# Kernel optimization log

Hardware: AMD Instinct MI355X
Metric: run time of the kernel (lower is better)

## Reference

```python
import jax, jax.numpy as jnp
import numpy as np

N_CLUSTERS = 1024


def setup_inputs() -> dict:
    key = jax.random.key(0)
    k1, k2 = jax.random.split(key)
    batch = jax.random.normal(k1, (262144, 64), dtype=jnp.float32)
    centroids = jax.random.normal(k2, (N_CLUSTERS, 64), dtype=jnp.float32)
    return {"batch": batch, "centroids": centroids}


def reference(batch, centroids):
    x_sq = jnp.sum(batch * batch, axis=1, keepdims=True)          # [N, 1]
    c_sq = jnp.sum(centroids * centroids, axis=1)                 # [K]
    cross = batch @ centroids.T                                   # [N, K]
    distances = x_sq - 2.0 * cross + c_sq[None, :]
    assignments = jnp.argmin(distances, axis=1)                   # [N] int
    # Counts and sums via scatter-add (avoids materializing one-hot [N, K])
    batch_cluster_counts = jnp.zeros((N_CLUSTERS,), dtype=jnp.int32).at[assignments].add(1)
    batch_cluster_sums = jax.ops.segment_sum(batch, assignments, num_segments=N_CLUSTERS)  # [K, D]
    return (assignments, batch_cluster_counts, batch_cluster_sums)
```

## Files before the change

kernel.cpp:

```cpp
#include <hip/hip_runtime.h>
#include <float.h>

#define N_PTS 262144
#define K_CL  1024
#define D     64
#define PTS_PER_WAVE   64
#define WAVES_PER_BLK  16
#define PTS_PER_BLK    (PTS_PER_WAVE * WAVES_PER_BLK)
#define NTILE 8
#define MARGIN_S 0.5f
#define CAND_CAP 6

typedef _Float16 f16;
typedef _Float16 half8 __attribute__((ext_vector_type(8)));
typedef float    f32x4 __attribute__((ext_vector_type(4)));

__global__ __launch_bounds__(256) void prep_kernel(const float* __restrict__ cent,
                                                   float* __restrict__ csq,
                                                   float* __restrict__ csqhn,
                                                   f16* __restrict__ cent16) {
    int k = blockIdx.x * 256 + threadIdx.x;
    if (k >= K_CL) return;
    const float* row = &cent[(size_t)k * D];
    float s = 0.f;
    #pragma unroll
    for (int d = 0; d < D; ++d) s = fmaf(row[d], row[d], s);
    csq[k]   = s;
    csqhn[k] = -0.5f * s;
    int sw = k & 7;
    #pragma unroll
    for (int ch = 0; ch < 8; ++ch) {
        half8 h;
        #pragma unroll
        for (int e = 0; e < 8; ++e) h[e] = (f16)row[ch * 8 + e];
        *reinterpret_cast<half8*>(&cent16[(size_t)k * D + (size_t)((ch ^ sw) * 8)]) = h;
    }
}

__device__ __forceinline__ float exact_dist(const float* __restrict__ xr,
                                            const float* __restrict__ cr,
                                            float xsq, float cs) {
    float dot = 0.f;
    #pragma unroll
    for (int d = 0; d < D; ++d) dot = fmaf(xr[d], cr[d], dot);
    return (xsq - 2.0f * dot) + cs;
}

__device__ __forceinline__ half8 point_frag(const float* __restrict__ batch,
                                            int prow, int chunk) {
    const float* src = &batch[(size_t)prow * D + chunk * 8];
    float4 u0 = *reinterpret_cast<const float4*>(src);
    float4 u1 = *reinterpret_cast<const float4*>(src + 4);
    half8 h;
    h[0] = (f16)u0.x; h[1] = (f16)u0.y; h[2] = (f16)u0.z; h[3] = (f16)u0.w;
    h[4] = (f16)u1.x; h[5] = (f16)u1.y; h[6] = (f16)u1.z; h[7] = (f16)u1.w;
    return h;
}

__device__ __forceinline__ float vmax4(const f32x4& a) {
    return fmaxf(fmaxf(a.x, a.y), fmaxf(a.z, a.w));
}

__device__ __forceinline__ void collect(const f32x4& a, float thr, int cbase, int& cnt,
                                        int& s0, int& s1, int& s2, int& s3, int& s4, int& s5) {
    if (vmax4(a) >= thr) {
        #pragma unroll
        for (int r = 0; r < 4; ++r) {
            if (a[r] >= thr) {
                int c = cbase + r;
                if      (cnt == 0) s0 = c;
                else if (cnt == 1) s1 = c;
                else if (cnt == 2) s2 = c;
                else if (cnt == 3) s3 = c;
                else if (cnt == 4) s4 = c;
                else if (cnt == 5) s5 = c;
                cnt++;
            }
        }
    }
}

__device__ __forceinline__ void resolve(const float* __restrict__ batch,
                                        const float* __restrict__ cent,
                                        const float* __restrict__ csq,
                                        int prow, int hi, int cnt,
                                        int s0, int s1, int s2, int s3, int s4, int s5,
                                        float& bd, int& bi) {
    bd = FLT_MAX; bi = 0x7fffffff;
    if (cnt == 0) return;
    const float* xr = &batch[(size_t)prow * D];
    float xsq = 0.f;
    #pragma unroll
    for (int d = 0; d < D; ++d) xsq = fmaf(xr[d], xr[d], xsq);
    if (cnt <= CAND_CAP) {
        #pragma unroll
        for (int r = 0; r < CAND_CAP; ++r) {
            int c = (r == 0) ? s0 : (r == 1) ? s1 : (r == 2) ? s2
                  : (r == 3) ? s3 : (r == 4) ? s4 : s5;
            if (r < cnt) {
                float dd = exact_dist(xr, &cent[(size_t)c * D], xsq, csq[c]);
                if (dd < bd || (dd == bd && c < bi)) { bd = dd; bi = c; }
            }
        }
    } else {
        for (int t16 = 0; t16 < 64; ++t16) {
            #pragma unroll
            for (int r = 0; r < 4; ++r) {
                int c = t16 * 16 + hi * 4 + r;
                float dd = exact_dist(xr, &cent[(size_t)c * D], xsq, csq[c]);
                if (dd < bd || (dd == bd && c < bi)) { bd = dd; bi = c; }
            }
        }
    }
}

__global__ __launch_bounds__(1024, 4) void assign_kernel(
    const float* __restrict__ batch,
    const f16*   __restrict__ cent16,
    const float* __restrict__ csq,
    const float* __restrict__ csqhn,
    const float* __restrict__ cent,
    float* __restrict__ out_assign,
    float* __restrict__ ps_base,
    float* __restrict__ cs_base,
    int split_mask)
{
    __shared__ f16   C16[K_CL * D];
    __shared__ __align__(16) float CH[K_CL];

    const int tid   = threadIdx.x;
    const int wave  = tid >> 6;
    const int lane  = tid & 63;
    const int lo    = lane & 15;
    const int hi    = lane >> 4;
    const int wbase = (blockIdx.x * WAVES_PER_BLK + wave) * PTS_PER_WAVE;

    #pragma unroll
    for (int it = 0; it < 8; ++it) {
        int u = tid + 1024 * it;
        *reinterpret_cast<half8*>(&C16[u * 8]) =
            *reinterpret_cast<const half8*>(&cent16[(size_t)u * 8]);
    }
    CH[tid] = csqhn[tid];
    __syncthreads();

    const int pr0 = wbase + 0 * 16 + lo;
    const int pr1 = wbase + 1 * 16 + lo;
    const int pr2 = wbase + 2 * 16 + lo;
    const int pr3 = wbase + 3 * 16 + lo;

    const half8 p0a = point_frag(batch, pr0, hi), p0b = point_frag(batch, pr0, 4 + hi);
    const half8 p1a = point_frag(batch, pr1, hi), p1b = point_frag(batch, pr1, 4 + hi);
    const half8 p2a = point_frag(batch, pr2, hi), p2b = point_frag(batch, pr2, 4 + hi);
    const half8 p3a = point_frag(batch, pr3, hi), p3b = point_frag(batch, pr3, 4 + hi);

    float m0 = -FLT_MAX, m1 = -FLT_MAX, m2 = -FLT_MAX, m3 = -FLT_MAX;
    for (int t = 0; t < NTILE; ++t) {
        const int base = t * 128;
        #pragma unroll
        for (int m = 0; m < 8; ++m) {
            const int row = base + m * 16 + lo;
            const int sw  = row & 7;
            const half8 cf0 = *reinterpret_cast<const half8*>(&C16[row * D + ((hi     ^ sw) * 8)]);
            const half8 cf1 = *reinterpret_cast<const half8*>(&C16[row * D + (((4+hi) ^ sw) * 8)]);
            const f32x4 ch  = *reinterpret_cast<const f32x4*>(&CH[base + m * 16 + hi * 4]);
            f32x4 a0 = ch, a1 = ch, a2 = ch, a3 = ch;
            a0 = __builtin_amdgcn_mfma_f32_16x16x32_f16(cf0, p0a, a0, 0, 0, 0);
            a0 = __builtin_amdgcn_mfma_f32_16x16x32_f16(cf1, p0b, a0, 0, 0, 0);
            a1 = __builtin_amdgcn_mfma_f32_16x16x32_f16(cf0, p1a, a1, 0, 0, 0);
            a1 = __builtin_amdgcn_mfma_f32_16x16x32_f16(cf1, p1b, a1, 0, 0, 0);
            a2 = __builtin_amdgcn_mfma_f32_16x16x32_f16(cf0, p2a, a2, 0, 0, 0);
            a2 = __builtin_amdgcn_mfma_f32_16x16x32_f16(cf1, p2b, a2, 0, 0, 0);
            a3 = __builtin_amdgcn_mfma_f32_16x16x32_f16(cf0, p3a, a3, 0, 0, 0);
            a3 = __builtin_amdgcn_mfma_f32_16x16x32_f16(cf1, p3b, a3, 0, 0, 0);
            m0 = fmaxf(m0, vmax4(a0));
            m1 = fmaxf(m1, vmax4(a1));
            m2 = fmaxf(m2, vmax4(a2));
            m3 = fmaxf(m3, vmax4(a3));
        }
    }
    m0 = fmaxf(m0, __shfl_xor(m0, 16)); m0 = fmaxf(m0, __shfl_xor(m0, 32));
    m1 = fmaxf(m1, __shfl_xor(m1, 16)); m1 = fmaxf(m1, __shfl_xor(m1, 32));
    m2 = fmaxf(m2, __shfl_xor(m2, 16)); m2 = fmaxf(m2, __shfl_xor(m2, 32));
    m3 = fmaxf(m3, __shfl_xor(m3, 16)); m3 = fmaxf(m3, __shfl_xor(m3, 32));
    const float t0 = m0 - MARGIN_S, t1 = m1 - MARGIN_S,
                t2 = m2 - MARGIN_S, t3 = m3 - MARGIN_S;

    int n0 = 0, n1 = 0, n2 = 0, n3 = 0;
    int a0c0=0,a0c1=0,a0c2=0,a0c3=0,a0c4=0,a0c5=0;
    int a1c0=0,a1c1=0,a1c2=0,a1c3=0,a1c4=0,a1c5=0;
    int a2c0=0,a2c1=0,a2c2=0,a2c3=0,a2c4=0,a2c5=0;
    int a3c0=0,a3c1=0,a3c2=0,a3c3=0,a3c4=0,a3c5=0;

    for (int t = 0; t < NTILE; ++t) {
        const int base = t * 128;
        #pragma unroll
        for (int m = 0; m < 8; ++m) {
            const int row = base + m * 16 + lo;
            const int sw  = row & 7;
            const half8 cf0 = *reinterpret_cast<const half8*>(&C16[row * D + ((hi     ^ sw) * 8)]);
            const half8 cf1 = *reinterpret_cast<const half8*>(&C16[row * D + (((4+hi) ^ sw) * 8)]);
            const f32x4 ch  = *reinterpret_cast<const f32x4*>(&CH[base + m * 16 + hi * 4]);
            f32x4 a0 = ch, a1 = ch, a2 = ch, a3 = ch;
            a0 = __builtin_amdgcn_mfma_f32_16x16x32_f16(cf0, p0a, a0, 0, 0, 0);
            a0 = __builtin_amdgcn_mfma_f32_16x16x32_f16(cf1, p0b, a0, 0, 0, 0);
            a1 = __builtin_amdgcn_mfma_f32_16x16x32_f16(cf0, p1a, a1, 0, 0, 0);
            a1 = __builtin_amdgcn_mfma_f32_16x16x32_f16(cf1, p1b, a1, 0, 0, 0);
            a2 = __builtin_amdgcn_mfma_f32_16x16x32_f16(cf0, p2a, a2, 0, 0, 0);
            a2 = __builtin_amdgcn_mfma_f32_16x16x32_f16(cf1, p2b, a2, 0, 0, 0);
            a3 = __builtin_amdgcn_mfma_f32_16x16x32_f16(cf0, p3a, a3, 0, 0, 0);
            a3 = __builtin_amdgcn_mfma_f32_16x16x32_f16(cf1, p3b, a3, 0, 0, 0);
            const int cbase = base + m * 16 + hi * 4;
            collect(a0, t0, cbase, n0, a0c0, a0c1, a0c2, a0c3, a0c4, a0c5);
            collect(a1, t1, cbase, n1, a1c0, a1c1, a1c2, a1c3, a1c4, a1c5);
            collect(a2, t2, cbase, n2, a2c0, a2c1, a2c2, a2c3, a2c4, a2c5);
            collect(a3, t3, cbase, n3, a3c0, a3c1, a3c2, a3c3, a3c4, a3c5);
        }
    }

    float bd0, bd1, bd2, bd3;
    int   bi0, bi1, bi2, bi3;
    resolve(batch, cent, csq, pr0, hi, n0, a0c0, a0c1, a0c2, a0c3, a0c4, a0c5, bd0, bi0);
    resolve(batch, cent, csq, pr1, hi, n1, a1c0, a1c1, a1c2, a1c3, a1c4, a1c5, bd1, bi1);
    resolve(batch, cent, csq, pr2, hi, n2, a2c0, a2c1, a2c2, a2c3, a2c4, a2c5, bd2, bi2);
    resolve(batch, cent, csq, pr3, hi, n3, a3c0, a3c1, a3c2, a3c3, a3c4, a3c5, bd3, bi3);

    #pragma unroll
    for (int off = 16; off <= 32; off <<= 1) {
        float od; int oi;
        od = __shfl_xor(bd0, off); oi = __shfl_xor(bi0, off);
        if (od < bd0 || (od == bd0 && oi < bi0)) { bd0 = od; bi0 = oi; }
        od = __shfl_xor(bd1, off); oi = __shfl_xor(bi1, off);
        if (od < bd1 || (od == bd1 && oi < bi1)) { bd1 = od; bi1 = oi; }
        od = __shfl_xor(bd2, off); oi = __shfl_xor(bi2, off);
        if (od < bd2 || (od == bd2 && oi < bi2)) { bd2 = od; bi2 = oi; }
        od = __shfl_xor(bd3, off); oi = __shfl_xor(bi3, off);
        if (od < bd3 || (od == bd3 && oi < bi3)) { bd3 = od; bi3 = oi; }
    }

    if (hi == 0) {
        out_assign[pr0] = (float)bi0;
        out_assign[pr1] = (float)bi1;
        out_assign[pr2] = (float)bi2;
        out_assign[pr3] = (float)bi3;
    }

    const int split = (blockIdx.x * WAVES_PER_BLK + wave) & split_mask;
    float* ps = ps_base + (size_t)split * K_CL * D;
    float* cs = cs_base + (size_t)split * K_CL;
    #pragma unroll 4
    for (int s = 0; s < 4; ++s) {
        int bis = (s == 0) ? bi0 : (s == 1) ? bi1 : (s == 2) ? bi2 : bi3;
        for (int p = 0; p < 16; ++p) {
            int a = __shfl(bis, p);
            int pt = wbase + s * 16 + p;
            float v = batch[(size_t)pt * D + lane];
            atomicAdd(&ps[(size_t)a * D + lane], v);
            if (lane == 0) atomicAdd(&cs[a], 1.0f);
        }
    }
}

__global__ __launch_bounds__(256) void reduce_kernel(
    const float* __restrict__ partial,
    const float* __restrict__ cnt_partial,
    float* __restrict__ out_counts,
    float* __restrict__ out_sums,
    int nsplit)
{
    int idx = blockIdx.x * 256 + threadIdx.x;
    if (idx < K_CL * D) {
        float s = 0.f;
        for (int e = 0; e < nsplit; ++e) s += partial[(size_t)e * K_CL * D + idx];
        out_sums[idx] = s;
    } else if (idx < K_CL * D + K_CL) {
        int c = idx - K_CL * D;
        float s = 0.f;
        for (int e = 0; e < nsplit; ++e) s += cnt_partial[e * K_CL + c];
        out_counts[c] = s;
    }
}

extern "C" void kernel_launch(void* const* d_in, const int* in_sizes, int n_in,
                              void* d_out, int out_size, void* d_ws, size_t ws_size,
                              hipStream_t stream) {
    const float* batch = (const float*)d_in[0];
    const float* cent  = (const float*)d_in[1];
    float* out        = (float*)d_out;
    float* out_assign = out;
    float* out_counts = out + N_PTS;
    float* out_sums   = out + N_PTS + K_CL;

    char* ws = (char*)d_ws;
    float* csq    = (float*)ws;
    float* csqhn  = (float*)(ws + 4096);
    f16*   cent16 = (f16*)(ws + 8192);
    float* partial = (float*)(ws + 8192 + 131072);

    int nsplit = 0;
    for (int ns = 32; ns >= 2; ns >>= 1) {
        size_t need = 8192 + 131072 +
                      (size_t)ns * K_CL * D * 4 + (size_t)ns * K_CL * 4;
        if (ws_size >= need) { nsplit = ns; break; }
    }

    prep_kernel<<<K_CL / 256, 256, 0, stream>>>(cent, csq, csqhn, cent16);

    if (nsplit > 0) {
        float* cnt_partial = partial + (size_t)nsplit * K_CL * D;
        hipMemsetAsync(partial, 0,
                       (size_t)(nsplit * K_CL * D + nsplit * K_CL) * sizeof(float), stream);
        assign_kernel<<<N_PTS / PTS_PER_BLK, 1024, 0, stream>>>(
            batch, cent16, csq, csqhn, cent, out_assign,
            partial, cnt_partial, nsplit - 1);
        reduce_kernel<<<(K_CL * D + K_CL + 255) / 256, 256, 0, stream>>>(
            partial, cnt_partial, out_counts, out_sums, nsplit);
    } else {
        hipMemsetAsync(out_counts, 0, (size_t)(K_CL + K_CL * D) * sizeof(float), stream);
        assign_kernel<<<N_PTS / PTS_PER_BLK, 1024, 0, stream>>>(
            batch, cent16, csq, csqhn, cent, out_assign,
            out_sums, out_counts, 0);
    }
}
```

Before: 191.0 us.

## Fuse max and candidate passes into one MFMA sweep with running top-4

```diff
diff --git a/kernel.cpp b/kernel.cpp
--- a/kernel.cpp
+++ b/kernel.cpp
@@ -9,7 +9,7 @@
 #define PTS_PER_BLK    (PTS_PER_WAVE * WAVES_PER_BLK)
 #define NTILE 8
 #define MARGIN_S 0.5f
-#define CAND_CAP 6
+#define CAP 4
 
 typedef _Float16 f16;
 typedef _Float16 half8 __attribute__((ext_vector_type(8)));
@@ -61,42 +61,50 @@
     return fmaxf(fmaxf(a.x, a.y), fmaxf(a.z, a.w));
 }
 
-__device__ __forceinline__ void collect(const f32x4& a, float thr, int cbase, int& cnt,
-                                        int& s0, int& s1, int& s2, int& s3, int& s4, int& s5) {
-    if (vmax4(a) >= thr) {
-        #pragma unroll
-        for (int r = 0; r < 4; ++r) {
-            if (a[r] >= thr) {
-                int c = cbase + r;
-                if      (cnt == 0) s0 = c;
-                else if (cnt == 1) s1 = c;
-                else if (cnt == 2) s2 = c;
-                else if (cnt == 3) s3 = c;
-                else if (cnt == 4) s4 = c;
-                else if (cnt == 5) s5 = c;
-                cnt++;
-            }
-        }
-    }
-}
-
-__device__ __forceinline__ void resolve(const float* __restrict__ batch,
-                                        const float* __restrict__ cent,
-                                        const float* __restrict__ csq,
-                                        int prow, int hi, int cnt,
-                                        int s0, int s1, int s2, int s3, int s4, int s5,
-                                        float& bd, int& bi) {
+__device__ __forceinline__ void rins(float sv, int c, int& cnt,
+                                     float& s0, float& s1, float& s2, float& s3,
+                                     int& i0, int& i1, int& i2, int& i3) {
+    if (cnt < CAP) {
+        if      (cnt == 0) { s0 = sv; i0 = c; }
+        else if (cnt == 1) { s1 = sv; i1 = c; }
+        else if (cnt == 2) { s2 = sv; i2 = c; }
+        else               { s3 = sv; i3 = c; }
+        cnt++;
+    } else {
+        float mn = s0; int mi = 0;
+        if (s1 < mn) { mn = s1; mi = 1; }
+        if (s2 < mn) { mn = s2; mi = 2; }
+        if (s3 < mn) { mn = s3; mi = 3; }
+        if (sv > mn) {
+            if      (mi == 0) { s0 = sv; i0 = c; }
+            else if (mi == 1) { s1 = sv; i1 = c; }
+            else if (mi == 2) { s2 = sv; i2 = c; }
+            else              { s3 = sv; i3 = c; }
+        }
+    }
+}
+
+__device__ __forceinline__ void resolve_r(const float* __restrict__ batch,
+                                          const float* __restrict__ cent,
+                                          const float* __restrict__ csq,
+                                          int prow, int hi, float thrF, int cnt,
+                                          float s0, float s1, float s2, float s3,
+                                          int i0, int i1, int i2, int i3,
+                                          float& bd, int& bi) {
     bd = FLT_MAX; bi = 0x7fffffff;
-    if (cnt == 0) return;
     const float* xr = &batch[(size_t)prow * D];
     float xsq = 0.f;
     #pragma unroll
     for (int d = 0; d < D; ++d) xsq = fmaf(xr[d], xr[d], xsq);
-    if (cnt <= CAND_CAP) {
+    int svc = 0;
+    if (cnt > 0 && s0 >= thrF) svc++;
+    if (cnt > 1 && s1 >= thrF) svc++;
+    if (cnt > 2 && s2 >= thrF) svc++;
+    if (cnt > 3 && s3 >= thrF) svc++;
+    if (svc < CAP) {
         #pragma unroll
-        for (int r = 0; r < CAND_CAP; ++r) {
-            int c = (r == 0) ? s0 : (r == 1) ? s1 : (r == 2) ? s2
-                  : (r == 3) ? s3 : (r == 4) ? s4 : s5;
+        for (int r = 0; r < CAP; ++r) {
+            int c = (r == 0) ? i0 : (r == 1) ? i1 : (r == 2) ? i2 : i3;
             if (r < cnt) {
                 float dd = exact_dist(xr, &cent[(size_t)c * D], xsq, csq[c]);
                 if (dd < bd || (dd == bd && c < bi)) { bd = dd; bi = c; }
@@ -155,42 +163,11 @@
     const half8 p3a = point_frag(batch, pr3, hi), p3b = point_frag(batch, pr3, 4 + hi);
 
     float m0 = -FLT_MAX, m1 = -FLT_MAX, m2 = -FLT_MAX, m3 = -FLT_MAX;
-    for (int t = 0; t < NTILE; ++t) {
-        const int base = t * 128;
-        #pragma unroll
-        for (int m = 0; m < 8; ++m) {
-            const int row = base + m * 16 + lo;
-            const int sw  = row & 7;
-            const half8 cf0 = *reinterpret_cast<const half8*>(&C16[row * D + ((hi     ^ sw) * 8)]);
-            const half8 cf1 = *reinterpret_cast<const half8*>(&C16[row * D + (((4+hi) ^ sw) * 8)]);
-            const f32x4 ch  = *reinterpret_cast<const f32x4*>(&CH[base + m * 16 + hi * 4]);
-            f32x4 a0 = ch, a1 = ch, a2 = ch, a3 = ch;
-            a0 = __builtin_amdgcn_mfma_f32_16x16x32_f16(cf0, p0a, a0, 0, 0, 0);
-            a0 = __builtin_amdgcn_mfma_f32_16x16x32_f16(cf1, p0b, a0, 0, 0, 0);
-            a1 = __builtin_amdgcn_mfma_f32_16x16x32_f16(cf0, p1a, a1, 0, 0, 0);
-            a1 = __builtin_amdgcn_mfma_f32_16x16x32_f16(cf1, p1b, a1, 0, 0, 0);
-            a2 = __builtin_amdgcn_mfma_f32_16x16x32_f16(cf0, p2a, a2, 0, 0, 0);
-            a2 = __builtin_amdgcn_mfma_f32_16x16x32_f16(cf1, p2b, a2, 0, 0, 0);
-            a3 = __builtin_amdgcn_mfma_f32_16x16x32_f16(cf0, p3a, a3, 0, 0, 0);
-            a3 = __builtin_amdgcn_mfma_f32_16x16x32_f16(cf1, p3b, a3, 0, 0, 0);
-            m0 = fmaxf(m0, vmax4(a0));
-            m1 = fmaxf(m1, vmax4(a1));
-            m2 = fmaxf(m2, vmax4(a2));
-            m3 = fmaxf(m3, vmax4(a3));
-        }
-    }
-    m0 = fmaxf(m0, __shfl_xor(m0, 16)); m0 = fmaxf(m0, __shfl_xor(m0, 32));
-    m1 = fmaxf(m1, __shfl_xor(m1, 16)); m1 = fmaxf(m1, __shfl_xor(m1, 32));
-    m2 = fmaxf(m2, __shfl_xor(m2, 16)); m2 = fmaxf(m2, __shfl_xor(m2, 32));
-    m3 = fmaxf(m3, __shfl_xor(m3, 16)); m3 = fmaxf(m3, __shfl_xor(m3, 32));
-    const float t0 = m0 - MARGIN_S, t1 = m1 - MARGIN_S,
-                t2 = m2 - MARGIN_S, t3 = m3 - MARGIN_S;
-
-    int n0 = 0, n1 = 0, n2 = 0, n3 = 0;
-    int a0c0=0,a0c1=0,a0c2=0,a0c3=0,a0c4=0,a0c5=0;
-    int a1c0=0,a1c1=0,a1c2=0,a1c3=0,a1c4=0,a1c5=0;
-    int a2c0=0,a2c1=0,a2c2=0,a2c3=0,a2c4=0,a2c5=0;
-    int a3c0=0,a3c1=0,a3c2=0,a3c3=0,a3c4=0,a3c5=0;
+    int   n0 = 0, n1 = 0, n2 = 0, n3 = 0;
+    float s00=0,s01=0,s02=0,s03=0, s10=0,s11=0,s12=0,s13=0;
+    float s20=0,s21=0,s22=0,s23=0, s30=0,s31=0,s32=0,s33=0;
+    int   i00=0,i01=0,i02=0,i03=0, i10=0,i11=0,i12=0,i13=0;
+    int   i20=0,i21=0,i22=0,i23=0, i30=0,i31=0,i32=0,i33=0;
 
     for (int t = 0; t < NTILE; ++t) {
         const int base = t * 128;
@@ -211,19 +188,62 @@
             a3 = __builtin_amdgcn_mfma_f32_16x16x32_f16(cf0, p3a, a3, 0, 0, 0);
             a3 = __builtin_amdgcn_mfma_f32_16x16x32_f16(cf1, p3b, a3, 0, 0, 0);
             const int cbase = base + m * 16 + hi * 4;
-            collect(a0, t0, cbase, n0, a0c0, a0c1, a0c2, a0c3, a0c4, a0c5);
-            collect(a1, t1, cbase, n1, a1c0, a1c1, a1c2, a1c3, a1c4, a1c5);
-            collect(a2, t2, cbase, n2, a2c0, a2c1, a2c2, a2c3, a2c4, a2c5);
-            collect(a3, t3, cbase, n3, a3c0, a3c1, a3c2, a3c3, a3c4, a3c5);
-        }
-    }
+
+            float mx;
+            mx = vmax4(a0); m0 = fmaxf(m0, mx);
+            if (mx >= m0 - MARGIN_S) {
+                #pragma unroll
+                for (int r = 0; r < 4; ++r) {
+                    float sv = a0[r];
+                    if (sv >= m0 - MARGIN_S)
+                        rins(sv, cbase + r, n0, s00, s01, s02, s03, i00, i01, i02, i03);
+                }
+            }
+            mx = vmax4(a1); m1 = fmaxf(m1, mx);
+            if (mx >= m1 - MARGIN_S) {
+                #pragma unroll
+                for (int r = 0; r < 4; ++r) {
+                    float sv = a1[r];
+                    if (sv >= m1 - MARGIN_S)
+                        rins(sv, cbase + r, n1, s10, s11, s12, s13, i10, i11, i12, i13);
+                }
+            }
+            mx = vmax4(a2); m2 = fmaxf(m2, mx);
+            if (mx >= m2 - MARGIN_S) {
+                #pragma unroll
+                for (int r = 0; r < 4; ++r) {
+                    float sv = a2[r];
+                    if (sv >= m2 - MARGIN_S)
+                        rins(sv, cbase + r, n2, s20, s21, s22, s23, i20, i21, i22, i23);
+                }
+            }
+            mx = vmax4(a3); m3 = fmaxf(m3, mx);
+            if (mx >= m3 - MARGIN_S) {
+                #pragma unroll
+                for (int r = 0; r < 4; ++r) {
+                    float sv = a3[r];
+                    if (sv >= m3 - MARGIN_S)
+                        rins(sv, cbase + r, n3, s30, s31, s32, s33, i30, i31, i32, i33);
+                }
+            }
+        }
+    }
+
+    m0 = fmaxf(m0, __shfl_xor(m0, 16)); m0 = fmaxf(m0, __shfl_xor(m0, 32));
+    m1 = fmaxf(m1, __shfl_xor(m1, 16)); m1 = fmaxf(m1, __shfl_xor(m1, 32));
+    m2 = fmaxf(m2, __shfl_xor(m2, 16)); m2 = fmaxf(m2, __shfl_xor(m2, 32));
+    m3 = fmaxf(m3, __shfl_xor(m3, 16)); m3 = fmaxf(m3, __shfl_xor(m3, 32));
 
     float bd0, bd1, bd2, bd3;
     int   bi0, bi1, bi2, bi3;
-    resolve(batch, cent, csq, pr0, hi, n0, a0c0, a0c1, a0c2, a0c3, a0c4, a0c5, bd0, bi0);
-    resolve(batch, cent, csq, pr1, hi, n1, a1c0, a1c1, a1c2, a1c3, a1c4, a1c5, bd1, bi1);
-    resolve(batch, cent, csq, pr2, hi, n2, a2c0, a2c1, a2c2, a2c3, a2c4, a2c5, bd2, bi2);
-    resolve(batch, cent, csq, pr3, hi, n3, a3c0, a3c1, a3c2, a3c3, a3c4, a3c5, bd3, bi3);
+    resolve_r(batch, cent, csq, pr0, hi, m0 - MARGIN_S, n0,
+              s00, s01, s02, s03, i00, i01, i02, i03, bd0, bi0);
+    resolve_r(batch, cent, csq, pr1, hi, m1 - MARGIN_S, n1,
+              s10, s11, s12, s13, i10, i11, i12, i13, bd1, bi1);
+    resolve_r(batch, cent, csq, pr2, hi, m2 - MARGIN_S, n2,
+              s20, s21, s22, s23, i20, i21, i22, i23, bd2, bi2);
+    resolve_r(batch, cent, csq, pr3, hi, m3 - MARGIN_S, n3,
+              s30, s31, s32, s33, i30, i31, i32, i33, bd3, bi3);
 
     #pragma unroll
     for (int off = 16; off <= 32; off <<= 1) {
@@ -308,7 +328,7 @@
 
     if (nsplit > 0) {
         float* cnt_partial = partial + (size_t)nsplit * K_CL * D;
-        hipMemsetAsync(partial, 0,
+        (void)hipMemsetAsync(partial, 0,
                        (size_t)(nsplit * K_CL * D + nsplit * K_CL) * sizeof(float), stream);
         assign_kernel<<<N_PTS / PTS_PER_BLK, 1024, 0, stream>>>(
             batch, cent16, csq, csqhn, cent, out_assign,
@@ -316,7 +336,7 @@
         reduce_kernel<<<(K_CL * D + K_CL + 255) / 256, 256, 0, stream>>>(
             partial, cnt_partial, out_counts, out_sums, nsplit);
     } else {
-        hipMemsetAsync(out_counts, 0, (size_t)(K_CL + K_CL * D) * sizeof(float), stream);
+        (void)hipMemsetAsync(out_counts, 0, (size_t)(K_CL + K_CL * D) * sizeof(float), stream);
         assign_kernel<<<N_PTS / PTS_PER_BLK, 1024, 0, stream>>>(
             batch, cent16, csq, csqhn, cent, out_assign,
             out_sums, out_counts, 0);
```

Measured after the change: 658.9 us. +245.0%, slower.

## Move cluster sum scatter into separate LDS-accumulating kernel, drop split partials

Applied to the files above, without the earlier changes.

```diff
diff --git a/kernel.cpp b/kernel.cpp
--- a/kernel.cpp
+++ b/kernel.cpp
@@ -10,6 +10,8 @@
 #define NTILE 8
 #define MARGIN_S 0.5f
 #define CAND_CAP 6
+#define SBLK 64
+#define PPB  (N_PTS / SBLK)
 
 typedef _Float16 f16;
 typedef _Float16 half8 __attribute__((ext_vector_type(8)));
@@ -120,10 +122,7 @@
     const float* __restrict__ csq,
     const float* __restrict__ csqhn,
     const float* __restrict__ cent,
-    float* __restrict__ out_assign,
-    float* __restrict__ ps_base,
-    float* __restrict__ cs_base,
-    int split_mask)
+    float* __restrict__ out_assign)
 {
     __shared__ f16   C16[K_CL * D];
     __shared__ __align__(16) float CH[K_CL];
@@ -244,41 +243,83 @@
         out_assign[pr2] = (float)bi2;
         out_assign[pr3] = (float)bi3;
     }
-
-    const int split = (blockIdx.x * WAVES_PER_BLK + wave) & split_mask;
-    float* ps = ps_base + (size_t)split * K_CL * D;
-    float* cs = cs_base + (size_t)split * K_CL;
-    #pragma unroll 4
-    for (int s = 0; s < 4; ++s) {
-        int bis = (s == 0) ? bi0 : (s == 1) ? bi1 : (s == 2) ? bi2 : bi3;
-        for (int p = 0; p < 16; ++p) {
-            int a = __shfl(bis, p);
-            int pt = wbase + s * 16 + p;
-            float v = batch[(size_t)pt * D + lane];
-            atomicAdd(&ps[(size_t)a * D + lane], v);
-            if (lane == 0) atomicAdd(&cs[a], 1.0f);
-        }
-    }
-}
-
-__global__ __launch_bounds__(256) void reduce_kernel(
-    const float* __restrict__ partial,
-    const float* __restrict__ cnt_partial,
+}
+
+__global__ __launch_bounds__(1024) void scatter_lds_kernel(
+    const float* __restrict__ batch,
+    const float* __restrict__ assignF,
     float* __restrict__ out_counts,
-    float* __restrict__ out_sums,
-    int nsplit)
+    float* __restrict__ out_sums)
 {
-    int idx = blockIdx.x * 256 + threadIdx.x;
-    if (idx < K_CL * D) {
-        float s = 0.f;
-        for (int e = 0; e < nsplit; ++e) s += partial[(size_t)e * K_CL * D + idx];
-        out_sums[idx] = s;
-    } else if (idx < K_CL * D + K_CL) {
-        int c = idx - K_CL * D;
-        float s = 0.f;
-        for (int e = 0; e < nsplit; ++e) s += cnt_partial[e * K_CL + c];
-        out_counts[c] = s;
-    }
+    __shared__ f16 S16[K_CL * D];
+    __shared__ int acnt[K_CL];
+    __shared__ int a_lds[PPB];
+
+    const int tid  = threadIdx.x;
+    const int wave = tid >> 6;
+    const int lane = tid & 63;
+    const size_t pbase = (size_t)blockIdx.x * PPB;
+
+    #pragma unroll
+    for (int i = 0; i < 8; ++i) {
+        int4 z = {0, 0, 0, 0};
+        *reinterpret_cast<int4*>(&S16[(tid + 1024 * i) * 8]) = z;
+    }
+    if (tid < K_CL) acnt[tid] = 0;
+    #pragma unroll
+    for (int i = 0; i < 4; ++i) {
+        int pl = tid + 1024 * i;
+        a_lds[pl] = (int)assignF[pbase + pl];
+    }
+    __syncthreads();
+
+    for (int chunk = 0; chunk < PPB / 64; ++chunk) {
+        int a_l = a_lds[chunk * 64 + lane];
+        unsigned long long mask = __ballot((a_l >> 6) == wave);
+        while (mask) {
+            int bit = __builtin_ctzll(mask);
+            mask &= mask - 1;
+            int pp = chunk * 64 + bit;
+            int c  = __shfl(a_l, bit);
+            float v = batch[(pbase + pp) * D + lane];
+            S16[c * D + lane] = (f16)((float)S16[c * D + lane] + v);
+            if (lane == 0) acnt[c]++;
+        }
+    }
+    __syncthreads();
+
+    const int c0 = wave * 64;
+    for (int i = 0; i < 64; ++i) {
+        int c = c0 + i;
+        int n = acnt[c];
+        if (n > 0) {
+            atomicAdd(&out_sums[(size_t)c * D + lane], (float)S16[c * D + lane]);
+            if (lane == 0) atomicAdd(&out_counts[c], (float)n);
+        }
+    }
+}
+
+__global__ __launch_bounds__(256) void assign_bruteforce_kernel(
+    const float* __restrict__ batch,
+    const float* __restrict__ cent,
+    float* __restrict__ out_assign)
+{
+    const int p = blockIdx.x * 256 + threadIdx.x;
+    if (p >= N_PTS) return;
+    const float* xr = &batch[(size_t)p * D];
+    float xsq = 0.f;
+    #pragma unroll
+    for (int d = 0; d < D; ++d) xsq = fmaf(xr[d], xr[d], xsq);
+    float bd = FLT_MAX; int bi = 0;
+    for (int c = 0; c < K_CL; ++c) {
+        const float* cr = &cent[(size_t)c * D];
+        float dot = 0.f, cs = 0.f;
+        #pragma unroll
+        for (int d = 0; d < D; ++d) { dot = fmaf(xr[d], cr[d], dot); cs = fmaf(cr[d], cr[d], cs); }
+        float dd = (xsq - 2.0f * dot) + cs;
+        if (dd < bd) { bd = dd; bi = c; }
+    }
+    out_assign[p] = (float)bi;
 }
 
 extern "C" void kernel_launch(void* const* d_in, const int* in_sizes, int n_in,
@@ -295,30 +336,16 @@
     float* csq    = (float*)ws;
     float* csqhn  = (float*)(ws + 4096);
     f16*   cent16 = (f16*)(ws + 8192);
-    float* partial = (float*)(ws + 8192 + 131072);
-
-    int nsplit = 0;
-    for (int ns = 32; ns >= 2; ns >>= 1) {
-        size_t need = 8192 + 131072 +
-                      (size_t)ns * K_CL * D * 4 + (size_t)ns * K_CL * 4;
-        if (ws_size >= need) { nsplit = ns; break; }
-    }
-
-    prep_kernel<<<K_CL / 256, 256, 0, stream>>>(cent, csq, csqhn, cent16);
-
-    if (nsplit > 0) {
-        float* cnt_partial = partial + (size_t)nsplit * K_CL * D;
-        hipMemsetAsync(partial, 0,
-                       (size_t)(nsplit * K_CL * D + nsplit * K_CL) * sizeof(float), stream);
+    const size_t need = 8192 + 131072;
+
+    (void)hipMemsetAsync(out_counts, 0, (size_t)(K_CL + K_CL * D) * sizeof(float), stream);
+
+    if (ws_size >= need) {
+        prep_kernel<<<K_CL / 256, 256, 0, stream>>>(cent, csq, csqhn, cent16);
         assign_kernel<<<N_PTS / PTS_PER_BLK, 1024, 0, stream>>>(
-            batch, cent16, csq, csqhn, cent, out_assign,
-            partial, cnt_partial, nsplit - 1);
-        reduce_kernel<<<(K_CL * D + K_CL + 255) / 256, 256, 0, stream>>>(
-            partial, cnt_partial, out_counts, out_sums, nsplit);
+            batch, cent16, csq, csqhn, cent, out_assign);
     } else {
-        hipMemsetAsync(out_counts, 0, (size_t)(K_CL + K_CL * D) * sizeof(float), stream);
-        assign_kernel<<<N_PTS / PTS_PER_BLK, 1024, 0, stream>>>(
-            batch, cent16, csq, csqhn, cent, out_assign,
-            out_sums, out_counts, 0);
-    }
-}
+        assign_bruteforce_kernel<<<N_PTS / 256, 256, 0, stream>>>(batch, cent, out_assign);
+    }
+    scatter_lds_kernel<<<SBLK, 1024, 0, stream>>>(batch, out_assign, out_counts, out_sums);
+}
```

Result: slower. 281.6 us (+47.4%).

## Replace global atomic scatter with per-block LDS histograms and store-based reduction

Applied to the files above, without the earlier changes.

```diff
diff --git a/kernel.cpp b/kernel.cpp
--- a/kernel.cpp
+++ b/kernel.cpp
@@ -7,9 +7,11 @@
 #define PTS_PER_WAVE   64
 #define WAVES_PER_BLK  16
 #define PTS_PER_BLK    (PTS_PER_WAVE * WAVES_PER_BLK)
+#define NBLK (N_PTS / PTS_PER_BLK)
 #define NTILE 8
 #define MARGIN_S 0.5f
 #define CAND_CAP 6
+#define HKC (K_CL / 2)
 
 typedef _Float16 f16;
 typedef _Float16 half8 __attribute__((ext_vector_type(8)));
@@ -114,6 +116,7 @@
     }
 }
 
+template<int TAIL>
 __global__ __launch_bounds__(1024, 4) void assign_kernel(
     const float* __restrict__ batch,
     const f16*   __restrict__ cent16,
@@ -121,12 +124,13 @@
     const float* __restrict__ csqhn,
     const float* __restrict__ cent,
     float* __restrict__ out_assign,
-    float* __restrict__ ps_base,
+    void*  __restrict__ part,
     float* __restrict__ cs_base,
     int split_mask)
 {
-    __shared__ f16   C16[K_CL * D];
+    __shared__ __align__(16) f16   C16[K_CL * D];
     __shared__ __align__(16) float CH[K_CL];
+    __shared__ int acnt[K_CL];
 
     const int tid   = threadIdx.x;
     const int wave  = tid >> 6;
@@ -245,23 +249,107 @@
         out_assign[pr3] = (float)bi3;
     }
 
-    const int split = (blockIdx.x * WAVES_PER_BLK + wave) & split_mask;
-    float* ps = ps_base + (size_t)split * K_CL * D;
-    float* cs = cs_base + (size_t)split * K_CL;
-    #pragma unroll 4
-    for (int s = 0; s < 4; ++s) {
-        int bis = (s == 0) ? bi0 : (s == 1) ? bi1 : (s == 2) ? bi2 : bi3;
-        for (int p = 0; p < 16; ++p) {
-            int a = __shfl(bis, p);
-            int pt = wbase + s * 16 + p;
-            float v = batch[(size_t)pt * D + lane];
-            atomicAdd(&ps[(size_t)a * D + lane], v);
-            if (lane == 0) atomicAdd(&cs[a], 1.0f);
-        }
-    }
-}
-
-__global__ __launch_bounds__(256) void reduce_kernel(
+    if constexpr (TAIL == 0) {
+        float* ps = (float*)part + (size_t)((blockIdx.x * WAVES_PER_BLK + wave) & split_mask) * K_CL * D;
+        float* cs = cs_base + (size_t)((blockIdx.x * WAVES_PER_BLK + wave) & split_mask) * K_CL;
+        #pragma unroll 4
+        for (int s = 0; s < 4; ++s) {
+            int bis = (s == 0) ? bi0 : (s == 1) ? bi1 : (s == 2) ? bi2 : bi3;
+            for (int p = 0; p < 16; ++p) {
+                int a = __shfl(bis, p);
+                int pt = wbase + s * 16 + p;
+                float v = batch[(size_t)pt * D + lane];
+                atomicAdd(&ps[(size_t)a * D + lane], v);
+                if (lane == 0) atomicAdd(&cs[a], 1.0f);
+            }
+        }
+    } else {
+        __syncthreads();
+        float* T    = reinterpret_cast<float*>(C16);
+        int*   a_sh = reinterpret_cast<int*>(CH);
+        float4* T4  = reinterpret_cast<float4*>(T);
+        {
+            float4 z = {0.f, 0.f, 0.f, 0.f};
+            #pragma unroll
+            for (int i = 0; i < 8; ++i) T4[tid + 1024 * i] = z;
+        }
+        acnt[tid] = 0;
+        if (hi == 0) {
+            a_sh[wave * 64 + 0 * 16 + lo] = bi0;
+            a_sh[wave * 64 + 1 * 16 + lo] = bi1;
+            a_sh[wave * 64 + 2 * 16 + lo] = bi2;
+            a_sh[wave * 64 + 3 * 16 + lo] = bi3;
+        }
+        __syncthreads();
+
+        #pragma unroll 4
+        for (int p = 0; p < 64; ++p) {
+            int a = a_sh[wave * 64 + p];
+            if (lane == 0) atomicAdd(&acnt[a], 1);
+            if (a < HKC) {
+                float v = batch[(size_t)(wbase + p) * D + lane];
+                atomicAdd(&T[a * D + lane], v);
+            }
+        }
+        __syncthreads();
+
+        const size_t pb = (size_t)blockIdx.x * (K_CL * D);
+        if constexpr (TAIL == 2) {
+            float4* dst = reinterpret_cast<float4*>((float*)part + pb);
+            #pragma unroll
+            for (int i = 0; i < 8; ++i) dst[tid + 1024 * i] = T4[tid + 1024 * i];
+        } else {
+            half8* dst = reinterpret_cast<half8*>((f16*)part + pb);
+            #pragma unroll
+            for (int i = 0; i < 4; ++i) {
+                int u = tid + 1024 * i;
+                float4 x0 = T4[u * 2], x1 = T4[u * 2 + 1];
+                half8 h;
+                h[0] = (f16)x0.x; h[1] = (f16)x0.y; h[2] = (f16)x0.z; h[3] = (f16)x0.w;
+                h[4] = (f16)x1.x; h[5] = (f16)x1.y; h[6] = (f16)x1.z; h[7] = (f16)x1.w;
+                dst[u] = h;
+            }
+        }
+        cs_base[(size_t)blockIdx.x * K_CL + tid] = (float)acnt[tid];
+        __syncthreads();
+
+        {
+            float4 z = {0.f, 0.f, 0.f, 0.f};
+            #pragma unroll
+            for (int i = 0; i < 8; ++i) T4[tid + 1024 * i] = z;
+        }
+        __syncthreads();
+
+        #pragma unroll 4
+        for (int p = 0; p < 64; ++p) {
+            int a = a_sh[wave * 64 + p];
+            if (a >= HKC) {
+                float v = batch[(size_t)(wbase + p) * D + lane];
+                atomicAdd(&T[(a - HKC) * D + lane], v);
+            }
+        }
+        __syncthreads();
+
+        if constexpr (TAIL == 2) {
+            float4* dst = reinterpret_cast<float4*>((float*)part + pb + (size_t)HKC * D);
+            #pragma unroll
+            for (int i = 0; i < 8; ++i) dst[tid + 1024 * i] = T4[tid + 1024 * i];
+        } else {
+            half8* dst = reinterpret_cast<half8*>((f16*)part + pb + (size_t)HKC * D);
+            #pragma unroll
+            for (int i = 0; i < 4; ++i) {
+                int u = tid + 1024 * i;
+                float4 x0 = T4[u * 2], x1 = T4[u * 2 + 1];
+                half8 h;
+                h[0] = (f16)x0.x; h[1] = (f16)x0.y; h[2] = (f16)x0.z; h[3] = (f16)x0.w;
+                h[4] = (f16)x1.x; h[5] = (f16)x1.y; h[6] = (f16)x1.z; h[7] = (f16)x1.w;
+                dst[u] = h;
+            }
+        }
+    }
+}
+
+__global__ __launch_bounds__(256) void reduce_atomic_kernel(
     const float* __restrict__ partial,
     const float* __restrict__ cnt_partial,
     float* __restrict__ out_counts,
@@ -281,6 +369,32 @@
     }
 }
 
+template<int TAIL>
+__global__ __launch_bounds__(256) void reduce_store_kernel(
+    const void* __restrict__ part,
+    const float* __restrict__ cnt_partial,
+    float* __restrict__ out_counts,
+    float* __restrict__ out_sums)
+{
+    int idx = blockIdx.x * 256 + threadIdx.x;
+    if (idx < K_CL * D) {
+        float s = 0.f;
+        if constexpr (TAIL == 2) {
+            const float* p = (const float*)part;
+            for (int b = 0; b < NBLK; ++b) s += p[(size_t)b * K_CL * D + idx];
+        } else {
+            const f16* p = (const f16*)part;
+            for (int b = 0; b < NBLK; ++b) s += (float)p[(size_t)b * K_CL * D + idx];
+        }
+        out_sums[idx] = s;
+    } else if (idx < K_CL * D + K_CL) {
+        int c = idx - K_CL * D;
+        float s = 0.f;
+        for (int b = 0; b < NBLK; ++b) s += cnt_partial[(size_t)b * K_CL + c];
+        out_counts[c] = s;
+    }
+}
+
 extern "C" void kernel_launch(void* const* d_in, const int* in_sizes, int n_in,
                               void* d_out, int out_size, void* d_ws, size_t ws_size,
                               hipStream_t stream) {
@@ -295,30 +409,45 @@
     float* csq    = (float*)ws;
     float* csqhn  = (float*)(ws + 4096);
     f16*   cent16 = (f16*)(ws + 8192);
-    float* partial = (float*)(ws + 8192 + 131072);
-
-    int nsplit = 0;
-    for (int ns = 32; ns >= 2; ns >>= 1) {
-        size_t need = 8192 + 131072 +
-                      (size_t)ns * K_CL * D * 4 + (size_t)ns * K_CL * 4;
-        if (ws_size >= need) { nsplit = ns; break; }
-    }
+    char*  part   = ws + 8192 + 131072;
+
+    const size_t base_need = 8192 + 131072;
+    const size_t cnt_bytes = (size_t)NBLK * K_CL * 4;
+    const size_t need_f32  = base_need + (size_t)NBLK * K_CL * D * 4 + cnt_bytes;
+    const size_t need_f16  = base_need + (size_t)NBLK * K_CL * D * 2 + cnt_bytes;
 
     prep_kernel<<<K_CL / 256, 256, 0, stream>>>(cent, csq, csqhn, cent16);
 
-    if (nsplit > 0) {
-        float* cnt_partial = partial + (size_t)nsplit * K_CL * D;
-        hipMemsetAsync(partial, 0,
-                       (size_t)(nsplit * K_CL * D + nsplit * K_CL) * sizeof(float), stream);
-        assign_kernel<<<N_PTS / PTS_PER_BLK, 1024, 0, stream>>>(
-            batch, cent16, csq, csqhn, cent, out_assign,
-            partial, cnt_partial, nsplit - 1);
-        reduce_kernel<<<(K_CL * D + K_CL + 255) / 256, 256, 0, stream>>>(
-            partial, cnt_partial, out_counts, out_sums, nsplit);
+    if (ws_size >= need_f32) {
+        float* cnts = (float*)(part + (size_t)NBLK * K_CL * D * 4);
+        assign_kernel<2><<<NBLK, 1024, 0, stream>>>(
+            batch, cent16, csq, csqhn, cent, out_assign, part, cnts, 0);
+        reduce_store_kernel<2><<<(K_CL * D + K_CL + 255) / 256, 256, 0, stream>>>(
+            part, cnts, out_counts, out_sums);
+    } else if (ws_size >= need_f16) {
+        float* cnts = (float*)(part + (size_t)NBLK * K_CL * D * 2);
+        assign_kernel<1><<<NBLK, 1024, 0, stream>>>(
+            batch, cent16, csq, csqhn, cent, out_assign, part, cnts, 0);
+        reduce_store_kernel<1><<<(K_CL * D + K_CL + 255) / 256, 256, 0, stream>>>(
+            part, cnts, out_counts, out_sums);
     } else {
-        hipMemsetAsync(out_counts, 0, (size_t)(K_CL + K_CL * D) * sizeof(float), stream);
-        assign_kernel<<<N_PTS / PTS_PER_BLK, 1024, 0, stream>>>(
-            batch, cent16, csq, csqhn, cent, out_assign,
-            out_sums, out_counts, 0);
-    }
-}
+        int nsplit = 0;
+        for (int ns = 32; ns >= 2; ns >>= 1) {
+            size_t need = base_need + (size_t)ns * K_CL * D * 4 + (size_t)ns * K_CL * 4;
+            if (ws_size >= need) { nsplit = ns; break; }
+        }
+        if (nsplit > 0) {
+            float* cnts = (float*)(part + (size_t)nsplit * K_CL * D * 4);
+            (void)hipMemsetAsync(part, 0,
+                    (size_t)nsplit * K_CL * D * 4 + (size_t)nsplit * K_CL * 4, stream);
+            assign_kernel<0><<<NBLK, 1024, 0, stream>>>(
+                batch, cent16, csq, csqhn, cent, out_assign, part, cnts, nsplit - 1);
+            reduce_atomic_kernel<<<(K_CL * D + K_CL + 255) / 256, 256, 0, stream>>>(
+                (float*)part, cnts, out_counts, out_sums, nsplit);
+        } else {
+            (void)hipMemsetAsync(out_counts, 0, (size_t)(K_CL + K_CL * D) * sizeof(float), stream);
+            assign_kernel<0><<<NBLK, 1024, 0, stream>>>(
+                batch, cent16, csq, csqhn, cent, out_assign, out_sums, out_counts, 0);
+        }
+    }
+}
```

New measurement: 215.2 us. +12.6%, slower.
